# Kernel optimization log

Measured on AMD Instinct MI355X. Metric: run time of the kernel, lower is better.

The kernel has to match this reference:

```python
import jax, jax.numpy as jnp
import numpy as np

MUL = 128          # multiplicity of each irrep (mul_in == mul_out)
DIMS = (1, 3, 5)   # ir dims for 0e, 1o, 2e
G = 32             # num_indices (weight groups)
N = 2048           # number of elements (rows)
W_FLAT = MUL * MUL * len(DIMS)


def setup_inputs() -> dict:
    key = jax.random.key(0)
    k0, k1, k2, kw = jax.random.split(key, 4)
    x0 = jax.random.normal(k0, (N, MUL, DIMS[0]), jnp.float32)
    x1 = jax.random.normal(k1, (N, MUL, DIMS[1]), jnp.float32)
    x2 = jax.random.normal(k2, (N, MUL, DIMS[2]), jnp.float32)
    w = jax.random.normal(kw, (G, W_FLAT), jnp.float32)
    # variable group sizes summing exactly to N (Repeats(num_index_counts))
    counts = np.random.default_rng(0).multinomial(N, np.ones(G) / G)
    repeats = jnp.asarray(counts, jnp.int32)
    return {"x0": x0, "x1": x1, "x2": x2, "w": w, "repeats": repeats}


def reference(x0, x1, x2, w, repeats):
    # Indexed equivariant linear: row n uses weight group seg[n], where the
    # first repeats[0] rows map to group 0, next repeats[1] rows to group 1, ...
    num_indices = w.shape[0]
    n = x0.shape[0]
    # scale/sqrt(num_indices) from the module times 1/sqrt(mul_in) path norm
    alpha = jnp.float32(1.0 / np.sqrt(num_indices * MUL))
    seg = jnp.searchsorted(jnp.cumsum(repeats), jnp.arange(n), side="right")
    outs = []
    off = 0
    for x in (x0, x1, x2):
        w_ir = w[:, off : off + MUL * MUL].reshape(num_indices, MUL, MUL)
        off += MUL * MUL
        w_el = w_ir[seg]  # (N, mul_in, mul_out) gathered per element
        # x: (N, mul_in, ir_dim) mul_ir layout -> y: (N, mul_out, ir_dim)
        y = jnp.einsum("nmi,nmo->noi", x, w_el) * alpha
        outs.append(y)
    return tuple(outs)
```

## Files before the change

kernel.cpp:

```cpp
#include <hip/hip_runtime.h>


#define NROWS 2048
#define NGROUP 32
#define WSTRIDE (128 * 128 * 3)
#define ALPHA 0.015625f

#define CAP0 96
#define CAP01 256
#define GRID_BLOCKS 544

template <int D, int TR, int RP, int SS>
__device__ inline void run_ir(int lt, const float* __restrict__ x,
                              const float* __restrict__ w_base_ir,
                              const int* __restrict__ repeats,
                              float* __restrict__ obase,
                              float (*Xs)[64], float (*Ws)[128]) {
  int off = 0, g = -1, row0 = 0, nr = 0;
  int tacc = 0;
  for (int gg = 0; gg < NGROUP; ++gg) {
    int c = repeats[gg];
    int tg = (c + TR - 1) / TR;
    if (lt < tacc + tg) {
      int tig = lt - tacc;
      g = gg;
      row0 = off + tig * TR;
      nr = min(TR, c - tig * TR);
      break;
    }
    tacc += tg;
    off += c;
  }
  if (g < 0) return;

  const int tid = threadIdx.x;
  const int to = tid & 31;
  const int tr = tid >> 5;

  constexpr int ROWELEMS = 128 * D;
  constexpr int BMELEMS = TR * ROWELEMS;
  const float* xrow = x + (size_t)row0 * ROWELEMS;
  for (int idx = tid; idx < BMELEMS; idx += 256) {
    int n_loc = idx / ROWELEMS;
    int rem = idx - n_loc * ROWELEMS;
    int m = rem / D;
    int i = rem - m * D;
    int rp = n_loc * D + i;
    int trp = rp / RP;
    int offp = rp - trp * RP;
    float v = 0.0f;
    if (n_loc < nr) v = xrow[idx];
    Xs[m][trp * SS + offp] = v;
  }

  const float* w_g = w_base_ir + (size_t)g * WSTRIDE;

  float acc[RP][4];
#pragma unroll
  for (int rr = 0; rr < RP; ++rr)
#pragma unroll
    for (int oj = 0; oj < 4; ++oj) acc[rr][oj] = 0.0f;

  for (int mt = 0; mt < 8; ++mt) {
    __syncthreads();
    {
      const float4* wsrc = (const float4*)(w_g + mt * 16 * 128);
      float4* wdst = (float4*)Ws;
      for (int idx = tid; idx < 512; idx += 256) wdst[idx] = wsrc[idx];
    }
    __syncthreads();
#pragma unroll
    for (int ml = 0; ml < 16; ++ml) {
      const int m = mt * 16 + ml;
      const float4 wf = *(const float4*)&Ws[ml][to * 4];
      float xs[RP];
#pragma unroll
      for (int rr = 0; rr < RP; ++rr) xs[rr] = Xs[m][tr * SS + rr];
#pragma unroll
      for (int rr = 0; rr < RP; ++rr) {
        acc[rr][0] += xs[rr] * wf.x;
        acc[rr][1] += xs[rr] * wf.y;
        acc[rr][2] += xs[rr] * wf.z;
        acc[rr][3] += xs[rr] * wf.w;
      }
    }
  }

#pragma unroll
  for (int rr = 0; rr < RP; ++rr) {
    int rp = tr * RP + rr;
    int n_loc = rp / D;
    int i = rp - n_loc * D;
    if (n_loc < nr) {
      float* orow = obase + (size_t)(row0 + n_loc) * ROWELEMS + i;
#pragma unroll
      for (int oj = 0; oj < 4; ++oj) orow[(to * 4 + oj) * D] = acc[rr][oj] * ALPHA;
    }
  }
}

__global__ __launch_bounds__(256) void IrrepsIndexedLinear_39161511805249_kernel(
    const float* __restrict__ x0, const float* __restrict__ x1,
    const float* __restrict__ x2, const float* __restrict__ w,
    const int* __restrict__ repeats, float* __restrict__ out) {
  __shared__ float Xs[128][64];
  __shared__ float Ws[16][128];

  const int bid = blockIdx.x;
  if (bid < CAP0) {
    run_ir<1, 32, 4, 4>(bid, x0, w, repeats, out, Xs, Ws);
  } else if (bid < CAP01) {
    run_ir<3, 16, 6, 8>(bid - CAP0, x1, w + 16384, repeats, out + 262144, Xs, Ws);
  } else {
    run_ir<5, 8, 5, 8>(bid - CAP01, x2, w + 32768, repeats, out + 1048576, Xs, Ws);
  }
}

extern "C" void kernel_launch(void* const* d_in, const int* in_sizes, int n_in,
                              void* d_out, int out_size, void* d_ws, size_t ws_size,
                              hipStream_t stream) {
  const float* x0 = (const float*)d_in[0];
  const float* x1 = (const float*)d_in[1];
  const float* x2 = (const float*)d_in[2];
  const float* w = (const float*)d_in[3];
  const int* repeats = (const int*)d_in[4];
  float* out = (float*)d_out;

  IrrepsIndexedLinear_39161511805249_kernel<<<GRID_BLOCKS, 256, 0, stream>>>(
      x0, x1, x2, w, repeats, out);
}
```

Baseline: 99.38 us.

## Stage X as contiguous float4 copy and read weights directly from global

X tiles are now copied into LDS with a plain vectorized float4 copy in their native row layout instead of a scalar transposing scatter, and the inner loop indexes them with precomputed offsets. The weight tile staging through LDS, along with its per-chunk double barriers, is removed; each thread loads its float4 of weights straight from global or cache inside the m loop. This cuts the synchronization and LDS traffic for weights. In exchange, the weight loads rely on L1/L2 hits, and strided LDS reads of X (stride D) may cause bank conflicts.

```diff
diff --git a/kernel.cpp b/kernel.cpp
--- a/kernel.cpp
+++ b/kernel.cpp
@@ -1,7 +1,6 @@
 #include <hip/hip_runtime.h>
 
 
-#define NROWS 2048
 #define NGROUP 32
 #define WSTRIDE (128 * 128 * 3)
 #define ALPHA 0.015625f
@@ -10,12 +9,14 @@
 #define CAP01 256
 #define GRID_BLOCKS 544
 
-template <int D, int TR, int RP, int SS>
+#define LDS_FLOATS 6144
+
+template <int D, int TR, int RP>
 __device__ inline void run_ir(int lt, const float* __restrict__ x,
                               const float* __restrict__ w_base_ir,
                               const int* __restrict__ repeats,
                               float* __restrict__ obase,
-                              float (*Xs)[64], float (*Ws)[128]) {
+                              float* __restrict__ Xs) {
   int off = 0, g = -1, row0 = 0, nr = 0;
   int tacc = 0;
   for (int gg = 0; gg < NGROUP; ++gg) {
@@ -39,21 +40,32 @@
 
   constexpr int ROWELEMS = 128 * D;
   constexpr int BMELEMS = TR * ROWELEMS;
-  const float* xrow = x + (size_t)row0 * ROWELEMS;
-  for (int idx = tid; idx < BMELEMS; idx += 256) {
-    int n_loc = idx / ROWELEMS;
-    int rem = idx - n_loc * ROWELEMS;
-    int m = rem / D;
-    int i = rem - m * D;
-    int rp = n_loc * D + i;
-    int trp = rp / RP;
-    int offp = rp - trp * RP;
-    float v = 0.0f;
-    if (n_loc < nr) v = xrow[idx];
-    Xs[m][trp * SS + offp] = v;
+
+  {
+    const float4* xsrc = (const float4*)(x + (size_t)row0 * ROWELEMS);
+    float4* xdst = (float4*)Xs;
+    const int limit4 = nr * (ROWELEMS / 4);
+    constexpr int Q = BMELEMS / 4;
+    const float4 z = make_float4(0.f, 0.f, 0.f, 0.f);
+    for (int q = tid; q < Q; q += 256) xdst[q] = (q < limit4) ? xsrc[q] : z;
+  }
+  __syncthreads();
+
+  int xoff[RP];
+  int nloc[RP];
+  int iofr[RP];
+#pragma unroll
+  for (int rr = 0; rr < RP; ++rr) {
+    int r = tr * RP + rr;
+    int nl = r / D;
+    int i = r - nl * D;
+    nloc[rr] = nl;
+    iofr[rr] = i;
+    xoff[rr] = nl * ROWELEMS + i;
   }
 
   const float* w_g = w_base_ir + (size_t)g * WSTRIDE;
+  const float4* wp = (const float4*)w_g + to;
 
   float acc[RP][4];
 #pragma unroll
@@ -61,40 +73,28 @@
 #pragma unroll
     for (int oj = 0; oj < 4; ++oj) acc[rr][oj] = 0.0f;
 
-  for (int mt = 0; mt < 8; ++mt) {
-    __syncthreads();
-    {
-      const float4* wsrc = (const float4*)(w_g + mt * 16 * 128);
-      float4* wdst = (float4*)Ws;
-      for (int idx = tid; idx < 512; idx += 256) wdst[idx] = wsrc[idx];
-    }
-    __syncthreads();
+#pragma unroll 8
+  for (int m = 0; m < 128; ++m) {
+    const float4 wf = wp[m * 32];
+    float xs[RP];
 #pragma unroll
-    for (int ml = 0; ml < 16; ++ml) {
-      const int m = mt * 16 + ml;
-      const float4 wf = *(const float4*)&Ws[ml][to * 4];
-      float xs[RP];
+    for (int rr = 0; rr < RP; ++rr) xs[rr] = Xs[xoff[rr] + m * D];
 #pragma unroll
-      for (int rr = 0; rr < RP; ++rr) xs[rr] = Xs[m][tr * SS + rr];
-#pragma unroll
-      for (int rr = 0; rr < RP; ++rr) {
-        acc[rr][0] += xs[rr] * wf.x;
-        acc[rr][1] += xs[rr] * wf.y;
-        acc[rr][2] += xs[rr] * wf.z;
-        acc[rr][3] += xs[rr] * wf.w;
-      }
+    for (int rr = 0; rr < RP; ++rr) {
+      acc[rr][0] += xs[rr] * wf.x;
+      acc[rr][1] += xs[rr] * wf.y;
+      acc[rr][2] += xs[rr] * wf.z;
+      acc[rr][3] += xs[rr] * wf.w;
     }
   }
 
 #pragma unroll
   for (int rr = 0; rr < RP; ++rr) {
-    int rp = tr * RP + rr;
-    int n_loc = rp / D;
-    int i = rp - n_loc * D;
-    if (n_loc < nr) {
-      float* orow = obase + (size_t)(row0 + n_loc) * ROWELEMS + i;
+    if (nloc[rr] < nr) {
+      float* orow = obase + (size_t)(row0 + nloc[rr]) * ROWELEMS + iofr[rr];
 #pragma unroll
-      for (int oj = 0; oj < 4; ++oj) orow[(to * 4 + oj) * D] = acc[rr][oj] * ALPHA;
+      for (int oj = 0; oj < 4; ++oj)
+        orow[(to * 4 + oj) * D] = acc[rr][oj] * ALPHA;
     }
   }
 }
@@ -103,16 +103,15 @@
     const float* __restrict__ x0, const float* __restrict__ x1,
     const float* __restrict__ x2, const float* __restrict__ w,
     const int* __restrict__ repeats, float* __restrict__ out) {
-  __shared__ float Xs[128][64];
-  __shared__ float Ws[16][128];
+  __shared__ float Xs[LDS_FLOATS];
 
   const int bid = blockIdx.x;
   if (bid < CAP0) {
-    run_ir<1, 32, 4, 4>(bid, x0, w, repeats, out, Xs, Ws);
+    run_ir<1, 32, 4>(bid, x0, w, repeats, out, Xs);
   } else if (bid < CAP01) {
-    run_ir<3, 16, 6, 8>(bid - CAP0, x1, w + 16384, repeats, out + 262144, Xs, Ws);
+    run_ir<3, 16, 6>(bid - CAP0, x1, w + 16384, repeats, out + 262144, Xs);
   } else {
-    run_ir<5, 8, 5, 8>(bid - CAP01, x2, w + 32768, repeats, out + 1048576, Xs, Ws);
+    run_ir<5, 8, 5>(bid - CAP01, x2, w + 32768, repeats, out + 1048576, Xs);
   }
 }
 
```

Measured after the change: 94.29 us. -5.1%, faster.
